# Performance work log

Measured on AMD Instinct MI355X. Metric: run time of the kernel, lower is better.

## Reference

```python
import jax, jax.numpy as jnp
import numpy as np

NUM_HEADS = 8

def _mha(x, in_w, in_b, out_w, out_b):
    # x: [B, L, E]; in_w: [3E, E]; out_w: [E, E]
    B, L, E = x.shape
    H = NUM_HEADS
    Dh = E // H
    qkv = x @ in_w.T + in_b                      # [B, L, 3E]
    q, k, v = jnp.split(qkv, 3, axis=-1)
    # [B, H, L, Dh]
    q = q.reshape(B, L, H, Dh).transpose(0, 2, 1, 3)
    k = k.reshape(B, L, H, Dh).transpose(0, 2, 1, 3)
    v = v.reshape(B, L, H, Dh).transpose(0, 2, 1, 3)
    scale = 1.0 / jnp.sqrt(jnp.asarray(Dh, dtype=x.dtype))
    scores = jnp.einsum('bhld,bhsd->bhls', q, k) * scale   # [B, H, L, S]
    attn = jax.nn.softmax(scores, axis=-1)
    ctx = jnp.einsum('bhls,bhsd->bhld', attn, v)           # [B, H, L, Dh]
    ctx = ctx.transpose(0, 2, 1, 3).reshape(B, L, E)
    out = ctx @ out_w.T + out_b                             # [B, L, E]
    # PyTorch default average_attn_weights=True: mean over heads -> [B, L, S]
    weights = attn.mean(axis=1)
    return out, weights

def setup_inputs() -> dict:
    key = jax.random.key(0)
    ks = jax.random.split(key, 5)
    B, L, E = 4, 2048, 1024
    s = 0.02
    return {
        'hidden_states': jax.random.normal(ks[0], (B, L, E), dtype=jnp.float32),
        'in_proj_w': jax.random.normal(ks[1], (3 * E, E), dtype=jnp.float32) * s,
        'in_proj_b': jnp.zeros((3 * E,), dtype=jnp.float32),
        'out_proj_w': jax.random.normal(ks[2], (E, E), dtype=jnp.float32) * s,
        'out_proj_b': jnp.zeros((E,), dtype=jnp.float32),
        'dep_proj_w': jax.random.normal(ks[3], (E, E), dtype=jnp.float32) * s,
        'dep_proj_b': jnp.zeros((E,), dtype=jnp.float32),
    }

def reference(hidden_states, in_proj_w, in_proj_b, out_proj_w, out_proj_b, dep_proj_w, dep_proj_b):
    enhanced, attn_weights = _mha(hidden_states, in_proj_w, in_proj_b, out_proj_w, out_proj_b)
    # dependency_scores: mean over query dim then key dim -> [B]
    dependency_scores = attn_weights.mean(axis=1).mean(axis=-1)
    enhanced = enhanced @ dep_proj_w.T + dep_proj_b
    return dependency_scores, enhanced
```

## Files before the change

### kernel.cpp

```cpp
#include <hip/hip_runtime.h>


typedef __attribute__((ext_vector_type(8))) short short8;
typedef __attribute__((ext_vector_type(4))) float float4v;
typedef __attribute__((ext_vector_type(4))) int int4v;
typedef __attribute__((ext_vector_type(2))) unsigned uint2v;

__device__ inline ushort f2bf(float f) {
  union { float f; unsigned u; } v; v.f = f;
  unsigned u = v.u;
  return (ushort)((u + 0x7FFFu + ((u >> 16) & 1u)) >> 16);
}
__device__ inline float bf2f(ushort h) {
  union { unsigned u; float f; } v; v.u = ((unsigned)h) << 16;
  return v.f;
}
__device__ inline unsigned cvtpk(float lo, float hi) {
  unsigned r;
  asm("v_cvt_pk_bf16_f32 %0, %1, %2" : "=v"(r) : "v"(lo), "v"(hi));
  return r;
}

__global__ __launch_bounds__(256)
void cvt_all(const float* __restrict__ X, const float* __restrict__ Wi,
             const float* __restrict__ Wd,
             ushort* __restrict__ Xb, ushort* __restrict__ Wib,
             ushort* __restrict__ Wdb) {
  size_t i = ((size_t)blockIdx.x * 256 + threadIdx.x) * 8;
  const float* src; ushort* dst;
  if (i < 8388608)        { src = X  + i;              dst = Xb  + i; }
  else if (i < 11534336)  { src = Wi + (i - 8388608);  dst = Wib + (i - 8388608); }
  else                    { src = Wd + (i - 11534336); dst = Wdb + (i - 11534336); }
  float4v a = *(const float4v*)(src);
  float4v b = *(const float4v*)(src + 4);
  ushort o[8];
  o[0] = f2bf(a.x); o[1] = f2bf(a.y); o[2] = f2bf(a.z); o[3] = f2bf(a.w);
  o[4] = f2bf(b.x); o[5] = f2bf(b.y); o[6] = f2bf(b.z); o[7] = f2bf(b.w);
  *(int4v*)dst = *(const int4v*)o;
}

__global__ __launch_bounds__(256)
void cvtT(const float* __restrict__ Wo, ushort* __restrict__ WoT) {
  __shared__ ushort Ts[64 * 72];
  const int t = threadIdx.x;
  const int ct = blockIdx.x * 64, rt = blockIdx.y * 64;
#pragma unroll
  for (int i = 0; i < 4; i++) {
    const int row = i * 16 + (t >> 4), col4 = (t & 15) * 4;
    float4v v = *(const float4v*)(Wo + (size_t)(rt + row) * 1024 + ct + col4);
    ushort o[4] = {f2bf(v.x), f2bf(v.y), f2bf(v.z), f2bf(v.w)};
    *(uint2v*)(Ts + row * 72 + col4) = *(const uint2v*)o;
  }
  __syncthreads();
#pragma unroll
  for (int it = 0; it < 2; it++) {
    const int c = it * 256 + t;
    const int oc = c >> 3, r8 = (c & 7) * 8;
    ushort o[8];
#pragma unroll
    for (int j = 0; j < 8; j++) o[j] = Ts[(r8 + j) * 72 + oc];
    *(int4v*)(WoT + (size_t)(ct + oc) * 1024 + rt + r8) = *(const int4v*)o;
  }
}

__global__ __launch_bounds__(64)
void bck(const float* __restrict__ Wd, const float* __restrict__ bo,
         const float* __restrict__ bd, float* __restrict__ bc,
         float* __restrict__ dep) {
  const int row = blockIdx.x, lane = threadIdx.x;
  float s = 0.f;
#pragma unroll
  for (int i = 0; i < 4; i++) {
    const int j = i * 256 + lane * 4;
    float4v w = *(const float4v*)(Wd + (size_t)row * 1024 + j);
    float4v b = *(const float4v*)(bo + j);
    s += w.x * b.x + w.y * b.y + w.z * b.z + w.w * b.w;
  }
#pragma unroll
  for (int off = 1; off <= 32; off <<= 1) s += __shfl_xor(s, off);
  if (lane == 0) bc[row] = s + bd[row];
  if (row < 4 && lane == 1) dep[row] = 1.0f / 2048.0f;
}

template <bool OUT_BF16>
__global__ __launch_bounds__(256, 2)
void gemm_bt(const ushort* __restrict__ A, const ushort* __restrict__ W,
             const float* __restrict__ bias, void* __restrict__ Cv,
             int M, int N, int K) {
  __shared__ ushort As[128 * 32];
  __shared__ ushort Bs[128 * 32];
  const int t = threadIdx.x;
  const int w = t >> 6;
  const int lane = t & 63;
  const int m16 = lane & 15, quad = lane >> 4;
  const int bx = blockIdx.x, by = blockIdx.y;
  const int warpRow = w >> 1, warpCol = w & 1;

  const int srow = t >> 2;
  const int scol = (t & 3) * 8;
  const ushort* Aptr = A + (size_t)(by * 128) * K;
  const ushort* Wptr = W + (size_t)(bx * 128) * K;

  float4v zero4 = {0.f, 0.f, 0.f, 0.f};
  float4v acc[4][4];
#pragma unroll
  for (int i = 0; i < 4; i++)
#pragma unroll
    for (int j = 0; j < 4; j++) acc[i][j] = zero4;

  for (int k0 = 0; k0 < K; k0 += 32) {
    __syncthreads();
#pragma unroll
    for (int r = 0; r < 2; r++) {
      const ushort* g = Aptr + (size_t)(r * 64 + srow) * K + (k0 + scol);
      __builtin_amdgcn_global_load_lds(
          (const __attribute__((address_space(1))) void*)g,
          (__attribute__((address_space(3))) void*)(As + r * 2048 + t * 8),
          16, 0, 0);
    }
#pragma unroll
    for (int r = 0; r < 2; r++) {
      const ushort* g = Wptr + (size_t)(r * 64 + srow) * K + (k0 + scol);
      __builtin_amdgcn_global_load_lds(
          (const __attribute__((address_space(1))) void*)g,
          (__attribute__((address_space(3))) void*)(Bs + r * 2048 + t * 8),
          16, 0, 0);
    }
    __syncthreads();

    short8 af[4], bf[4];
#pragma unroll
    for (int i = 0; i < 4; i++) {
      af[i] = *(const short8*)(As + (warpRow * 64 + i * 16 + m16) * 32 + quad * 8);
      bf[i] = *(const short8*)(Bs + (warpCol * 64 + i * 16 + m16) * 32 + quad * 8);
    }
#pragma unroll
    for (int i = 0; i < 4; i++)
#pragma unroll
      for (int j = 0; j < 4; j++)
        acc[i][j] = __builtin_amdgcn_mfma_f32_16x16x32_bf16(af[i], bf[j],
                                                            acc[i][j], 0, 0, 0);
  }

  const int crow_base = by * 128 + warpRow * 64;
  const int ccol_base = bx * 128 + warpCol * 64;
#pragma unroll
  for (int j = 0; j < 4; j++) {
    const int col = ccol_base + j * 16 + m16;
    const float bv = bias ? bias[col] : 0.0f;
#pragma unroll
    for (int i = 0; i < 4; i++) {
      const int row = crow_base + i * 16 + quad * 4;
#pragma unroll
      for (int r = 0; r < 4; r++) {
        const float v = acc[i][j][r] + bv;
        if constexpr (OUT_BF16)
          ((ushort*)Cv)[(size_t)(row + r) * N + col] = f2bf(v);
        else
          ((float*)Cv)[(size_t)(row + r) * N + col] = v;
      }
    }
  }
}

__global__ __launch_bounds__(256, 2)
void gemm_qkv(const ushort* __restrict__ Xb, const ushort* __restrict__ Wib,
              const float* __restrict__ bi, ushort* __restrict__ qkv,
              ushort* __restrict__ Vt,
              const ushort* __restrict__ A2, const ushort* __restrict__ W2,
              ushort* __restrict__ C2) {
  __shared__ ushort As[128 * 32];
  __shared__ ushort Bs[128 * 32];
  const int t = threadIdx.x;
  const int w = t >> 6;
  const int lane = t & 63;
  const int m16 = lane & 15, quad = lane >> 4;
  const int bid = blockIdx.x;
  const bool second = bid >= 1536;
  int bx, by;
  const ushort *A, *W;
  if (!second) { bx = bid % 24; by = bid / 24; A = Xb; W = Wib; }
  else { const int b2 = bid - 1536; bx = b2 & 7; by = b2 >> 3; A = A2; W = W2; }
  const int warpRow = w >> 1, warpCol = w & 1;
  const int K = 1024;

  const int srow = t >> 2;
  const int scol = (t & 3) * 8;
  const ushort* Aptr = A + (size_t)(by * 128) * K;
  const ushort* Wptr = W + (size_t)(bx * 128) * K;

  float4v zero4 = {0.f, 0.f, 0.f, 0.f};
  float4v acc[4][4];
#pragma unroll
  for (int i = 0; i < 4; i++)
#pragma unroll
    for (int j = 0; j < 4; j++) acc[i][j] = zero4;

  for (int k0 = 0; k0 < K; k0 += 32) {
    __syncthreads();
#pragma unroll
    for (int r = 0; r < 2; r++) {
      const ushort* g = Aptr + (size_t)(r * 64 + srow) * K + (k0 + scol);
      __builtin_amdgcn_global_load_lds(
          (const __attribute__((address_space(1))) void*)g,
          (__attribute__((address_space(3))) void*)(As + r * 2048 + t * 8),
          16, 0, 0);
    }
#pragma unroll
    for (int r = 0; r < 2; r++) {
      const ushort* g = Wptr + (size_t)(r * 64 + srow) * K + (k0 + scol);
      __builtin_amdgcn_global_load_lds(
          (const __attribute__((address_space(1))) void*)g,
          (__attribute__((address_space(3))) void*)(Bs + r * 2048 + t * 8),
          16, 0, 0);
    }
    __syncthreads();

    short8 af[4], bf[4];
#pragma unroll
    for (int i = 0; i < 4; i++) {
      af[i] = *(const short8*)(As + (warpRow * 64 + i * 16 + m16) * 32 + quad * 8);
      bf[i] = *(const short8*)(Bs + (warpCol * 64 + i * 16 + m16) * 32 + quad * 8);
    }
#pragma unroll
    for (int i = 0; i < 4; i++)
#pragma unroll
      for (int j = 0; j < 4; j++)
        acc[i][j] = __builtin_amdgcn_mfma_f32_16x16x32_bf16(af[i], bf[j],
                                                            acc[i][j], 0, 0, 0);
  }

  const int crow_base = by * 128 + warpRow * 64;
  const int ccol_base = bx * 128 + warpCol * 64;

  if (second) {
#pragma unroll
    for (int j = 0; j < 4; j++) {
      const int col = ccol_base + j * 16 + m16;
#pragma unroll
      for (int i = 0; i < 4; i++) {
        const int row = crow_base + i * 16 + quad * 4;
#pragma unroll
        for (int r = 0; r < 4; r++)
          C2[(size_t)(row + r) * 1024 + col] = f2bf(acc[i][j][r]);
      }
    }
  } else if (bx < 16) {
#pragma unroll
    for (int j = 0; j < 4; j++) {
      const int col = ccol_base + j * 16 + m16;
      const float bv = bi[col];
#pragma unroll
      for (int i = 0; i < 4; i++) {
        const int row = crow_base + i * 16 + quad * 4;
#pragma unroll
        for (int r = 0; r < 4; r++)
          qkv[(size_t)(row + r) * 3072 + col] = f2bf(acc[i][j][r] + bv);
      }
    }
  } else {
    const int b = by >> 4;
#pragma unroll
    for (int j = 0; j < 4; j++) {
      const int col = ccol_base + j * 16 + m16;
      const float bv = bi[col];
      const int vcol = col - 2048;
      const int h = vcol >> 7, d = vcol & 127;
      ushort* vrow = Vt + (size_t)((b * 8 + h) * 128 + d) * 2048;
#pragma unroll
      for (int i = 0; i < 4; i++) {
        const int pos = ((by & 15) << 7) + warpRow * 64 + ((i >> 1) << 5) +
                        (2 * quad + (i & 1)) * 4;
        uint2v o;
        o.x = cvtpk(acc[i][j][0] + bv, acc[i][j][1] + bv);
        o.y = cvtpk(acc[i][j][2] + bv, acc[i][j][3] + bv);
        *(uint2v*)(vrow + pos) = o;
      }
    }
  }
}

__global__ __launch_bounds__(256, 2)
void attn(const ushort* __restrict__ qkv, const ushort* __restrict__ Vt,
          ushort* __restrict__ ctx) {
  __shared__ ushort Ks[4][32 * 128];
  __shared__ ushort Vsm[4][128 * 32];
  const int t = threadIdx.x, w = t >> 6, lane = t & 63;
  const int m16 = lane & 15, quad = lane >> 4;
  const int qt = blockIdx.x, h = blockIdx.y, b = blockIdx.z;
  const int E3 = 3072;
  const size_t bbase = (size_t)b * 2048;

  const ushort* Qg = qkv + (bbase + qt * 128 + w * 32) * E3 + h * 128;
  const ushort* Kg = qkv + bbase * E3 + 1024 + h * 128;
  const ushort* Vg = Vt + (size_t)((b * 8 + h) * 128) * 2048;

  auto stage = [&](int kt, int buf) {
#pragma unroll
    for (int it = 0; it < 2; it++) {
      const int c = it * 256 + t;
      const int row = c >> 4, cir = c & 15;
      const int j = (cir & 8) | ((cir ^ row) & 7);
      const ushort* g = Kg + (size_t)(kt * 32 + row) * E3 + j * 8;
      __builtin_amdgcn_global_load_lds(
          (const __attribute__((address_space(1))) void*)g,
          (__attribute__((address_space(3))) void*)(&Ks[buf][c * 8]), 16, 0, 0);
    }
#pragma unroll
    for (int it = 0; it < 2; it++) {
      const int c = it * 256 + t;
      const int d = c >> 2, cir = c & 3;
      const int j = cir ^ ((d >> 1) & 3);
      const ushort* g = Vg + (size_t)d * 2048 + kt * 32 + j * 8;
      __builtin_amdgcn_global_load_lds(
          (const __attribute__((address_space(1))) void*)g,
          (__attribute__((address_space(3))) void*)(&Vsm[buf][c * 8]), 16, 0, 0);
    }
  };

  stage(0, 0);
  stage(1, 1);

  const float c1 = 0.08838834764831845f * 1.4426950408889634f;
  short8 qf[2][4];
#pragma unroll
  for (int g = 0; g < 2; g++)
#pragma unroll
    for (int ks = 0; ks < 4; ks++) {
      short8 raw = *(const short8*)(Qg + (size_t)(g * 16 + m16) * E3 + ks * 32 + quad * 8);
      short8 s;
#pragma unroll
      for (int j = 0; j < 8; j++) s[j] = (short)f2bf(bf2f((ushort)raw[j]) * c1);
      qf[g][ks] = s;
    }

  int kslot[4];
#pragma unroll
  for (int ks = 0; ks < 4; ks++) {
    const int j = ks * 4 + quad;
    kslot[ks] = (j & 8) | ((j ^ m16) & 7);
  }
  const int vslot = quad ^ ((m16 >> 1) & 3);

  float4v zero4 = {0.f, 0.f, 0.f, 0.f};
  float4v Oacc[2][8];
#pragma unroll
  for (int g = 0; g < 2; g++)
#pragma unroll
    for (int dt = 0; dt < 8; dt++) Oacc[g][dt] = zero4;
  float lsum[2] = {0.f, 0.f};

  for (int kt = 0; kt < 64; kt++) {
    if (kt < 62) {
      stage(kt + 2, (kt + 2) & 3);
      asm volatile("s_waitcnt vmcnt(8)" ::: "memory");
    } else if (kt == 62) {
      asm volatile("s_waitcnt vmcnt(4)" ::: "memory");
    } else {
      asm volatile("s_waitcnt vmcnt(0)" ::: "memory");
    }
    __builtin_amdgcn_s_barrier();
    __builtin_amdgcn_sched_barrier(0);
    const ushort* Ksb = Ks[kt & 3];
    const ushort* Vsb = Vsm[kt & 3];

    float4v st[2][2];
    st[0][0] = zero4; st[0][1] = zero4; st[1][0] = zero4; st[1][1] = zero4;
    __builtin_amdgcn_s_setprio(1);
#pragma unroll
    for (int ks = 0; ks < 4; ks++) {
#pragma unroll
      for (int mt2 = 0; mt2 < 2; mt2++) {
        short8 kf = *(const short8*)(Ksb + (mt2 * 16 + m16) * 128 + kslot[ks] * 8);
        st[0][mt2] = __builtin_amdgcn_mfma_f32_16x16x32_bf16(kf, qf[0][ks], st[0][mt2], 0, 0, 0);
        st[1][mt2] = __builtin_amdgcn_mfma_f32_16x16x32_bf16(kf, qf[1][ks], st[1][mt2], 0, 0, 0);
      }
    }
    __builtin_amdgcn_s_setprio(0);

    short8 pfr[2];
#pragma unroll
    for (int g = 0; g < 2; g++) {
      unsigned pk[4];
#pragma unroll
      for (int mt2 = 0; mt2 < 2; mt2++) {
        float p0 = __builtin_exp2f(st[g][mt2][0]);
        float p1 = __builtin_exp2f(st[g][mt2][1]);
        float p2 = __builtin_exp2f(st[g][mt2][2]);
        float p3 = __builtin_exp2f(st[g][mt2][3]);
        lsum[g] += (p0 + p1) + (p2 + p3);
        pk[mt2 * 2]     = cvtpk(p0, p1);
        pk[mt2 * 2 + 1] = cvtpk(p2, p3);
      }
      union { int4v i; short8 s; } pf;
      pf.i.x = (int)pk[0];
      pf.i.y = (int)pk[1];
      pf.i.z = (int)pk[2];
      pf.i.w = (int)pk[3];
      pfr[g] = pf.s;
    }

    __builtin_amdgcn_s_setprio(1);
#pragma unroll
    for (int dt = 0; dt < 8; dt++) {
      short8 vf = *(const short8*)(Vsb + (dt * 16 + m16) * 32 + vslot * 8);
      Oacc[0][dt] = __builtin_amdgcn_mfma_f32_16x16x32_bf16(pfr[0], vf, Oacc[0][dt], 0, 0, 0);
      Oacc[1][dt] = __builtin_amdgcn_mfma_f32_16x16x32_bf16(pfr[1], vf, Oacc[1][dt], 0, 0, 0);
    }
    __builtin_amdgcn_s_setprio(0);
  }

#pragma unroll
  for (int g = 0; g < 2; g++) {
    float l = lsum[g];
    l += __shfl_xor(l, 16);
    l += __shfl_xor(l, 32);
    float* lf = (float*)(&Ks[0][w * 64]);
    lf[m16] = l;
    float linv[4];
#pragma unroll
    for (int r = 0; r < 4; r++) linv[r] = 1.0f / lf[quad * 4 + r];
#pragma unroll
    for (int r = 0; r < 4; r++) {
      const int row = qt * 128 + w * 32 + g * 16 + quad * 4 + r;
      ushort* crow = ctx + (bbase + row) * 1024 + h * 128;
#pragma unroll
      for (int dt = 0; dt < 8; dt++)
        crow[dt * 16 + m16] = f2bf(Oacc[g][dt][r] * linv[r]);
    }
  }
}

extern "C" void kernel_launch(void* const* d_in, const int* in_sizes, int n_in,
                              void* d_out, int out_size, void* d_ws, size_t ws_size,
                              hipStream_t stream) {
  const float* X  = (const float*)d_in[0];
  const float* Wi = (const float*)d_in[1];
  const float* bi = (const float*)d_in[2];
  const float* Wo = (const float*)d_in[3];
  const float* bo = (const float*)d_in[4];
  const float* Wd = (const float*)d_in[5];
  const float* bd = (const float*)d_in[6];
  float* out = (float*)d_out;

  ushort* p    = (ushort*)d_ws;
  ushort* Xb   = p; p += (size_t)8192 * 1024;
  ushort* Wib  = p; p += (size_t)3072 * 1024;
  ushort* WoTb = p; p += (size_t)1024 * 1024;
  ushort* Wdb  = p; p += (size_t)1024 * 1024;
  ushort* qkv  = p; p += (size_t)8192 * 3072;
  ushort* Vt   = p; p += (size_t)4096 * 2048;
  float*  bc   = (float*)p; p += 2048;
  ushort* WcbSep = p; p += (size_t)1024 * 1024;
  const size_t need_merged = (size_t)((char*)p - (char*)d_ws);
  const bool merged = ws_size >= need_merged;

  ushort* ctx = Xb;
  ushort* Wcb = merged ? WcbSep : Wib;

  cvt_all<<<6144, 256, 0, stream>>>(X, Wi, Wd, Xb, Wib, Wdb);
  cvtT<<<dim3(16, 16), 256, 0, stream>>>(Wo, WoTb);
  bck<<<1024, 64, 0, stream>>>(Wd, bo, bd, bc, out);
  if (merged) {
    gemm_qkv<<<1600, 256, 0, stream>>>(Xb, Wib, bi, qkv, Vt, Wdb, WoTb, Wcb);
  } else {
    gemm_qkv<<<1536, 256, 0, stream>>>(Xb, Wib, bi, qkv, Vt, Wdb, WoTb, nullptr);
    gemm_bt<true><<<dim3(8, 8), 256, 0, stream>>>(Wdb, WoTb, nullptr, Wcb,
                                                  1024, 1024, 1024);
  }
  attn<<<dim3(16, 8, 4), 256, 0, stream>>>(qkv, Vt, ctx);
  gemm_bt<false><<<dim3(8, 64), 256, 0, stream>>>(ctx, Wcb, bc, out + 4,
                                                  8192, 1024, 1024);
}
```

Baseline: 297.5 us.

## Merge prep kernels, swizzle GEMM block order, widen attention blocks to 512 threads

Three small conversion and bias kernels become one prep launch to cut launch overhead. The QKV and final GEMMs remap block indices so consecutive blocks spread across XCDs and share operand tiles in cache. Attention now uses 512-thread blocks covering 256 query rows, so each staged K/V tile serves twice as many queries, with per-thread staging and wait counts adjusted to match. The final GEMM becomes a dedicated kernel. The larger attention block lowers occupancy to one block per CU.

Result: faster. 287.3 us (-3.4%).

```diff
diff --git a/kernel.cpp b/kernel.cpp
--- a/kernel.cpp
+++ b/kernel.cpp
@@ -22,71 +22,69 @@
 }
 
 __global__ __launch_bounds__(256)
-void cvt_all(const float* __restrict__ X, const float* __restrict__ Wi,
-             const float* __restrict__ Wd,
-             ushort* __restrict__ Xb, ushort* __restrict__ Wib,
-             ushort* __restrict__ Wdb) {
-  size_t i = ((size_t)blockIdx.x * 256 + threadIdx.x) * 8;
-  const float* src; ushort* dst;
-  if (i < 8388608)        { src = X  + i;              dst = Xb  + i; }
-  else if (i < 11534336)  { src = Wi + (i - 8388608);  dst = Wib + (i - 8388608); }
-  else                    { src = Wd + (i - 11534336); dst = Wdb + (i - 11534336); }
-  float4v a = *(const float4v*)(src);
-  float4v b = *(const float4v*)(src + 4);
-  ushort o[8];
-  o[0] = f2bf(a.x); o[1] = f2bf(a.y); o[2] = f2bf(a.z); o[3] = f2bf(a.w);
-  o[4] = f2bf(b.x); o[5] = f2bf(b.y); o[6] = f2bf(b.z); o[7] = f2bf(b.w);
-  *(int4v*)dst = *(const int4v*)o;
-}
-
-__global__ __launch_bounds__(256)
-void cvtT(const float* __restrict__ Wo, ushort* __restrict__ WoT) {
+void prep(const float* __restrict__ X, const float* __restrict__ Wi,
+          const float* __restrict__ Wd, const float* __restrict__ Wo,
+          const float* __restrict__ bo, const float* __restrict__ bd,
+          ushort* __restrict__ Xb, ushort* __restrict__ Wib,
+          ushort* __restrict__ Wdb, ushort* __restrict__ WoT,
+          float* __restrict__ bc, float* __restrict__ dep) {
   __shared__ ushort Ts[64 * 72];
+  const int bid = blockIdx.x;
   const int t = threadIdx.x;
-  const int ct = blockIdx.x * 64, rt = blockIdx.y * 64;
-#pragma unroll
-  for (int i = 0; i < 4; i++) {
-    const int row = i * 16 + (t >> 4), col4 = (t & 15) * 4;
-    float4v v = *(const float4v*)(Wo + (size_t)(rt + row) * 1024 + ct + col4);
-    ushort o[4] = {f2bf(v.x), f2bf(v.y), f2bf(v.z), f2bf(v.w)};
-    *(uint2v*)(Ts + row * 72 + col4) = *(const uint2v*)o;
-  }
-  __syncthreads();
-#pragma unroll
-  for (int it = 0; it < 2; it++) {
-    const int c = it * 256 + t;
-    const int oc = c >> 3, r8 = (c & 7) * 8;
+
+  if (bid < 6144) {
+    size_t i = ((size_t)bid * 256 + t) * 8;
+    const float* src; ushort* dst;
+    if (i < 8388608)        { src = X  + i;              dst = Xb  + i; }
+    else if (i < 11534336)  { src = Wi + (i - 8388608);  dst = Wib + (i - 8388608); }
+    else                    { src = Wd + (i - 11534336); dst = Wdb + (i - 11534336); }
+    float4v a = *(const float4v*)(src);
+    float4v b = *(const float4v*)(src + 4);
     ushort o[8];
-#pragma unroll
-    for (int j = 0; j < 8; j++) o[j] = Ts[(r8 + j) * 72 + oc];
-    *(int4v*)(WoT + (size_t)(ct + oc) * 1024 + rt + r8) = *(const int4v*)o;
-  }
-}
-
-__global__ __launch_bounds__(64)
-void bck(const float* __restrict__ Wd, const float* __restrict__ bo,
-         const float* __restrict__ bd, float* __restrict__ bc,
-         float* __restrict__ dep) {
-  const int row = blockIdx.x, lane = threadIdx.x;
-  float s = 0.f;
-#pragma unroll
-  for (int i = 0; i < 4; i++) {
-    const int j = i * 256 + lane * 4;
-    float4v w = *(const float4v*)(Wd + (size_t)row * 1024 + j);
-    float4v b = *(const float4v*)(bo + j);
-    s += w.x * b.x + w.y * b.y + w.z * b.z + w.w * b.w;
-  }
-#pragma unroll
-  for (int off = 1; off <= 32; off <<= 1) s += __shfl_xor(s, off);
-  if (lane == 0) bc[row] = s + bd[row];
-  if (row < 4 && lane == 1) dep[row] = 1.0f / 2048.0f;
-}
-
-template <bool OUT_BF16>
+    o[0] = f2bf(a.x); o[1] = f2bf(a.y); o[2] = f2bf(a.z); o[3] = f2bf(a.w);
+    o[4] = f2bf(b.x); o[5] = f2bf(b.y); o[6] = f2bf(b.z); o[7] = f2bf(b.w);
+    *(int4v*)dst = *(const int4v*)o;
+  } else if (bid < 6400) {
+    const int q = bid - 6144;
+    const int ct = (q & 15) * 64, rt = (q >> 4) * 64;
+#pragma unroll
+    for (int i = 0; i < 4; i++) {
+      const int row = i * 16 + (t >> 4), col4 = (t & 15) * 4;
+      float4v v = *(const float4v*)(Wo + (size_t)(rt + row) * 1024 + ct + col4);
+      ushort o[4] = {f2bf(v.x), f2bf(v.y), f2bf(v.z), f2bf(v.w)};
+      *(uint2v*)(Ts + row * 72 + col4) = *(const uint2v*)o;
+    }
+    __syncthreads();
+#pragma unroll
+    for (int it = 0; it < 2; it++) {
+      const int c = it * 256 + t;
+      const int oc = c >> 3, r8 = (c & 7) * 8;
+      ushort o[8];
+#pragma unroll
+      for (int j = 0; j < 8; j++) o[j] = Ts[(r8 + j) * 72 + oc];
+      *(int4v*)(WoT + (size_t)(ct + oc) * 1024 + rt + r8) = *(const int4v*)o;
+    }
+  } else {
+    const int w = t >> 6, lane = t & 63;
+    const int row = (bid - 6400) * 4 + w;
+    float s = 0.f;
+#pragma unroll
+    for (int i = 0; i < 4; i++) {
+      const int j = i * 256 + lane * 4;
+      float4v wv = *(const float4v*)(Wd + (size_t)row * 1024 + j);
+      float4v bv = *(const float4v*)(bo + j);
+      s += wv.x * bv.x + wv.y * bv.y + wv.z * bv.z + wv.w * bv.w;
+    }
+#pragma unroll
+    for (int off = 1; off <= 32; off <<= 1) s += __shfl_xor(s, off);
+    if (lane == 0) bc[row] = s + bd[row];
+    if (row < 4 && lane == 1) dep[row] = 1.0f / 2048.0f;
+  }
+}
+
 __global__ __launch_bounds__(256, 2)
 void gemm_bt(const ushort* __restrict__ A, const ushort* __restrict__ W,
-             const float* __restrict__ bias, void* __restrict__ Cv,
-             int M, int N, int K) {
+             ushort* __restrict__ C, int K) {
   __shared__ ushort As[128 * 32];
   __shared__ ushort Bs[128 * 32];
   const int t = threadIdx.x;
@@ -147,18 +145,12 @@
 #pragma unroll
   for (int j = 0; j < 4; j++) {
     const int col = ccol_base + j * 16 + m16;
-    const float bv = bias ? bias[col] : 0.0f;
 #pragma unroll
     for (int i = 0; i < 4; i++) {
       const int row = crow_base + i * 16 + quad * 4;
 #pragma unroll
-      for (int r = 0; r < 4; r++) {
-        const float v = acc[i][j][r] + bv;
-        if constexpr (OUT_BF16)
-          ((ushort*)Cv)[(size_t)(row + r) * N + col] = f2bf(v);
-        else
-          ((float*)Cv)[(size_t)(row + r) * N + col] = v;
-      }
+      for (int r = 0; r < 4; r++)
+        C[(size_t)(row + r) * 1024 + col] = f2bf(acc[i][j][r]);
     }
   }
 }
@@ -179,8 +171,12 @@
   const bool second = bid >= 1536;
   int bx, by;
   const ushort *A, *W;
-  if (!second) { bx = bid % 24; by = bid / 24; A = Xb; W = Wib; }
-  else { const int b2 = bid - 1536; bx = b2 & 7; by = b2 >> 3; A = A2; W = W2; }
+  if (!second) {
+    const int swz = (bid & 7) * 192 + (bid >> 3);
+    bx = swz % 24; by = swz / 24; A = Xb; W = Wib;
+  } else {
+    const int b2 = bid - 1536; bx = b2 & 7; by = b2 >> 3; A = A2; W = W2;
+  }
   const int warpRow = w >> 1, warpCol = w & 1;
   const int K = 1024;
 
@@ -280,41 +276,41 @@
   }
 }
 
-__global__ __launch_bounds__(256, 2)
+__global__ __launch_bounds__(512, 1)
 void attn(const ushort* __restrict__ qkv, const ushort* __restrict__ Vt,
           ushort* __restrict__ ctx) {
   __shared__ ushort Ks[4][32 * 128];
   __shared__ ushort Vsm[4][128 * 32];
   const int t = threadIdx.x, w = t >> 6, lane = t & 63;
   const int m16 = lane & 15, quad = lane >> 4;
-  const int qt = blockIdx.x, h = blockIdx.y, b = blockIdx.z;
+  const int i = blockIdx.x;
+  const int x = i & 7, jj0 = i >> 3;
+  const int pair = x * 4 + (jj0 >> 3);
+  const int qt = jj0 & 7;
+  const int h = pair & 7, b = pair >> 3;
   const int E3 = 3072;
   const size_t bbase = (size_t)b * 2048;
 
-  const ushort* Qg = qkv + (bbase + qt * 128 + w * 32) * E3 + h * 128;
+  const ushort* Qg = qkv + (bbase + qt * 256 + w * 32) * E3 + h * 128;
   const ushort* Kg = qkv + bbase * E3 + 1024 + h * 128;
   const ushort* Vg = Vt + (size_t)((b * 8 + h) * 128) * 2048;
 
   auto stage = [&](int kt, int buf) {
-#pragma unroll
-    for (int it = 0; it < 2; it++) {
-      const int c = it * 256 + t;
-      const int row = c >> 4, cir = c & 15;
+    {
+      const int row = t >> 4, cir = t & 15;
       const int j = (cir & 8) | ((cir ^ row) & 7);
       const ushort* g = Kg + (size_t)(kt * 32 + row) * E3 + j * 8;
       __builtin_amdgcn_global_load_lds(
           (const __attribute__((address_space(1))) void*)g,
-          (__attribute__((address_space(3))) void*)(&Ks[buf][c * 8]), 16, 0, 0);
-    }
-#pragma unroll
-    for (int it = 0; it < 2; it++) {
-      const int c = it * 256 + t;
-      const int d = c >> 2, cir = c & 3;
+          (__attribute__((address_space(3))) void*)(&Ks[buf][t * 8]), 16, 0, 0);
+    }
+    {
+      const int d = t >> 2, cir = t & 3;
       const int j = cir ^ ((d >> 1) & 3);
       const ushort* g = Vg + (size_t)d * 2048 + kt * 32 + j * 8;
       __builtin_amdgcn_global_load_lds(
           (const __attribute__((address_space(1))) void*)g,
-          (__attribute__((address_space(3))) void*)(&Vsm[buf][c * 8]), 16, 0, 0);
+          (__attribute__((address_space(3))) void*)(&Vsm[buf][t * 8]), 16, 0, 0);
     }
   };
 
@@ -353,9 +349,9 @@
   for (int kt = 0; kt < 64; kt++) {
     if (kt < 62) {
       stage(kt + 2, (kt + 2) & 3);
-      asm volatile("s_waitcnt vmcnt(8)" ::: "memory");
+      asm volatile("s_waitcnt vmcnt(4)" ::: "memory");
     } else if (kt == 62) {
-      asm volatile("s_waitcnt vmcnt(4)" ::: "memory");
+      asm volatile("s_waitcnt vmcnt(2)" ::: "memory");
     } else {
       asm volatile("s_waitcnt vmcnt(0)" ::: "memory");
     }
@@ -422,11 +418,87 @@
     for (int r = 0; r < 4; r++) linv[r] = 1.0f / lf[quad * 4 + r];
 #pragma unroll
     for (int r = 0; r < 4; r++) {
-      const int row = qt * 128 + w * 32 + g * 16 + quad * 4 + r;
+      const int row = qt * 256 + w * 32 + g * 16 + quad * 4 + r;
       ushort* crow = ctx + (bbase + row) * 1024 + h * 128;
 #pragma unroll
       for (int dt = 0; dt < 8; dt++)
         crow[dt * 16 + m16] = f2bf(Oacc[g][dt][r] * linv[r]);
+    }
+  }
+}
+
+__global__ __launch_bounds__(256, 2)
+void gemm_fin(const ushort* __restrict__ A, const ushort* __restrict__ W,
+              const float* __restrict__ bias, float* __restrict__ C) {
+  __shared__ ushort As[128 * 32];
+  __shared__ ushort Bs[128 * 32];
+  const int t = threadIdx.x;
+  const int w = t >> 6;
+  const int lane = t & 63;
+  const int m16 = lane & 15, quad = lane >> 4;
+  const int swz = (blockIdx.x & 7) * 64 + (blockIdx.x >> 3);
+  const int bx = swz & 7, by = swz >> 3;
+  const int warpRow = w >> 1, warpCol = w & 1;
+  const int K = 1024;
+
+  const int srow = t >> 2;
+  const int scol = (t & 3) * 8;
+  const ushort* Aptr = A + (size_t)(by * 128) * K;
+  const ushort* Wptr = W + (size_t)(bx * 128) * K;
+
+  float4v zero4 = {0.f, 0.f, 0.f, 0.f};
+  float4v acc[4][4];
+#pragma unroll
+  for (int i = 0; i < 4; i++)
+#pragma unroll
+    for (int j = 0; j < 4; j++) acc[i][j] = zero4;
+
+  for (int k0 = 0; k0 < K; k0 += 32) {
+    __syncthreads();
+#pragma unroll
+    for (int r = 0; r < 2; r++) {
+      const ushort* g = Aptr + (size_t)(r * 64 + srow) * K + (k0 + scol);
+      __builtin_amdgcn_global_load_lds(
+          (const __attribute__((address_space(1))) void*)g,
+          (__attribute__((address_space(3))) void*)(As + r * 2048 + t * 8),
+          16, 0, 0);
+    }
+#pragma unroll
+    for (int r = 0; r < 2; r++) {
+      const ushort* g = Wptr + (size_t)(r * 64 + srow) * K + (k0 + scol);
+      __builtin_amdgcn_global_load_lds(
+          (const __attribute__((address_space(1))) void*)g,
+          (__attribute__((address_space(3))) void*)(Bs + r * 2048 + t * 8),
+          16, 0, 0);
+    }
+    __syncthreads();
+
+    short8 af[4], bf[4];
+#pragma unroll
+    for (int i = 0; i < 4; i++) {
+      af[i] = *(const short8*)(As + (warpRow * 64 + i * 16 + m16) * 32 + quad * 8);
+      bf[i] = *(const short8*)(Bs + (warpCol * 64 + i * 16 + m16) * 32 + quad * 8);
+    }
+#pragma unroll
+    for (int i = 0; i < 4; i++)
+#pragma unroll
+      for (int j = 0; j < 4; j++)
+        acc[i][j] = __builtin_amdgcn_mfma_f32_16x16x32_bf16(af[i], bf[j],
+                                                            acc[i][j], 0, 0, 0);
+  }
+
+  const int crow_base = by * 128 + warpRow * 64;
+  const int ccol_base = bx * 128 + warpCol * 64;
+#pragma unroll
+  for (int j = 0; j < 4; j++) {
+    const int col = ccol_base + j * 16 + m16;
+    const float bv = bias[col];
+#pragma unroll
+    for (int i = 0; i < 4; i++) {
+      const int row = crow_base + i * 16 + quad * 4;
+#pragma unroll
+      for (int r = 0; r < 4; r++)
+        C[(size_t)(row + r) * 1024 + col] = acc[i][j][r] + bv;
     }
   }
 }
@@ -458,17 +530,14 @@
   ushort* ctx = Xb;
   ushort* Wcb = merged ? WcbSep : Wib;
 
-  cvt_all<<<6144, 256, 0, stream>>>(X, Wi, Wd, Xb, Wib, Wdb);
-  cvtT<<<dim3(16, 16), 256, 0, stream>>>(Wo, WoTb);
-  bck<<<1024, 64, 0, stream>>>(Wd, bo, bd, bc, out);
+  prep<<<6656, 256, 0, stream>>>(X, Wi, Wd, Wo, bo, bd,
+                                 Xb, Wib, Wdb, WoTb, bc, out);
   if (merged) {
     gemm_qkv<<<1600, 256, 0, stream>>>(Xb, Wib, bi, qkv, Vt, Wdb, WoTb, Wcb);
   } else {
     gemm_qkv<<<1536, 256, 0, stream>>>(Xb, Wib, bi, qkv, Vt, Wdb, WoTb, nullptr);
-    gemm_bt<true><<<dim3(8, 8), 256, 0, stream>>>(Wdb, WoTb, nullptr, Wcb,
-                                                  1024, 1024, 1024);
-  }
-  attn<<<dim3(16, 8, 4), 256, 0, stream>>>(qkv, Vt, ctx);
-  gemm_bt<false><<<dim3(8, 64), 256, 0, stream>>>(ctx, Wcb, bc, out + 4,
-                                                  8192, 1024, 1024);
-}
+    gemm_bt<<<dim3(8, 8), 256, 0, stream>>>(Wdb, WoTb, Wcb, 1024);
+  }
+  attn<<<256, 512, 0, stream>>>(qkv, Vt, ctx);
+  gemm_fin<<<512, 256, 0, stream>>>(ctx, Wcb, bc, out + 4);
+}
```
